# Performance work log

Measured on AMD Instinct MI355X. Metric: run time of the kernel, lower is better.

The kernel has to match this reference:

```python
import jax, jax.numpy as jnp
import numpy as np

EPS = 1e-5
NUM_HEADS = 8


def _conv_transpose_3x3_s2(x, w):
    # x: [B,Cin,H,W], w: [Cin,Cout,3,3] (torch ConvTranspose2d layout), stride 2, no padding
    # output spatial = (H-1)*2 + 3 = 2H+1
    return jax.lax.conv_transpose(
        x, w, strides=(2, 2), padding='VALID',
        dimension_numbers=('NCHW', 'IOHW', 'NCHW'))


def setup_inputs() -> dict:
    key = jax.random.key(0)
    ks = jax.random.split(key, 8)
    B, C, H, W = 4, 256, 32, 32
    Co, Dk, Dv = 128, 64, 64
    s = 0.05
    return {
        'x': jax.random.normal(ks[0], (B, C, H, W), jnp.float32),
        'gamma': jnp.ones((C,), jnp.float32),
        'beta': jnp.zeros((C,), jnp.float32),
        'running_mean': jax.random.normal(ks[1], (C,), jnp.float32) * 0.1,
        'running_var': jax.random.uniform(ks[2], (C,), jnp.float32, 0.5, 1.5),
        'w_sc': jax.random.normal(ks[3], (C, Co, 3, 3), jnp.float32) * s,
        'w_q': jax.random.normal(ks[4], (C, Dk, 3, 3), jnp.float32) * s,
        'w_k': jax.random.normal(ks[5], (Dk, C), jnp.float32) * s,
        'w_v': jax.random.normal(ks[6], (Dv, C), jnp.float32) * s,
        'w_o': jax.random.normal(ks[7], (Co, Dv), jnp.float32) * s,
    }


def reference(x, gamma, beta, running_mean, running_var, w_sc, w_q, w_k, w_v, w_o):
    B, C, H, W = x.shape
    h = NUM_HEADS
    # BatchNorm (inference, running stats) + ReLU, shared by both branches
    inv = jax.lax.rsqrt(running_var + EPS)
    xn = (x - running_mean[None, :, None, None]) * (gamma * inv)[None, :, None, None] \
         + beta[None, :, None, None]
    xr = jax.nn.relu(xn)

    # Shortcut: ConvTranspose2d(C->Co, 3, stride 2) -> [B,Co,2H+1,2W+1]
    shortcut = _conv_transpose_3x3_s2(xr, w_sc)

    # Attention branch ('UP'): query upsampled via ConvTranspose, k/v 1x1 at low res
    q = _conv_transpose_3x3_s2(xr, w_q)              # [B,Dk,Hu,Wu]
    k = jnp.einsum('dc,bchw->bdhw', w_k, xr)         # [B,Dk,H,W]
    v = jnp.einsum('dc,bchw->bdhw', w_v, xr)         # [B,Dv,H,W]
    Hu, Wu = q.shape[2], q.shape[3]
    Nq, Nk = Hu * Wu, H * W
    Dk, Dv = q.shape[1], v.shape[1]
    dk = Dk // h
    qh = q.reshape(B, h, dk, Nq)
    kh = k.reshape(B, h, dk, Nk)
    vh = v.reshape(B, h, Dv // h, Nk)
    scores = jnp.einsum('bhdq,bhdk->bhqk', qh, kh) / jnp.sqrt(jnp.float32(dk))
    attn = jax.nn.softmax(scores, axis=-1)           # use_softmax=True
    out = jnp.einsum('bhqk,bhdk->bhdq', attn, vh)    # [B,h,dv,Nq]
    out = out.reshape(B, Dv, Hu, Wu)
    out = jnp.einsum('od,bdhw->bohw', w_o, out)      # 1x1 output projection -> Co

    return shortcut + out
```

## Files before the change

kernel.cpp:

```cpp
#include <hip/hip_runtime.h>

typedef unsigned short u16;
typedef unsigned int u32;

typedef float f4 __attribute__((ext_vector_type(4)));
typedef short s8v __attribute__((ext_vector_type(8)));
typedef u16 us8 __attribute__((ext_vector_type(8)));
typedef _Float16 h4 __attribute__((ext_vector_type(4)));
typedef __fp16 g2 __attribute__((ext_vector_type(2)));

__device__ __forceinline__ u16 f2bf(float x){ u32 b=__float_as_uint(x); b += 0x7FFFu + ((b>>16)&1u); return (u16)(b>>16); }
__device__ __forceinline__ u16 f2h(float x){ union{_Float16 h; u16 u;} c; c.h=(_Float16)x; return c.u; }

#define O_XRT  4096u
#define O_WPT  (O_XRT + 2367488u)
#define O_QH   (O_WPT + 884736u)
#define O_KT   (O_QH  + 2163200u)
#define O_V    (O_KT  + 524288u)
#define O_ATT  (O_V   + 524288u)
#define O_WKV  (O_ATT + 2163200u)
#define O_WO2  (O_WKV + 65536u)

__global__ __launch_bounds__(256) void k_prep(
    const float* __restrict__ x, const float* __restrict__ gamma, const float* __restrict__ beta,
    const float* __restrict__ mean, const float* __restrict__ var,
    const float* __restrict__ w_sc, const float* __restrict__ w_q,
    const float* __restrict__ w_k, const float* __restrict__ w_v, const float* __restrict__ w_o,
    u16* __restrict__ xrTp, u16* __restrict__ wpt,
    u16* __restrict__ wkv, u16* __restrict__ wo2)
{
  __shared__ float SS[128], SH[128];
  __shared__ __align__(16) u16 T[32*136];
  int bi = blockIdx.x, tid = threadIdx.x;
  if (bi < 256) {
    int b = bi >> 6, pt = (bi >> 1) & 31, ch = bi & 1;
    int pix0 = pt*32, c0 = ch*128;
    if (tid < 128) {
      int c = c0 + tid;
      float s = gamma[c]*rsqrtf(var[c] + 1e-5f);
      SS[tid] = s; SH[tid] = beta[c] - mean[c]*s;
    }
    __syncthreads();
    int pix_l = tid & 31, c_l = tid >> 5;
    #pragma unroll 4
    for (int it = 0; it < 16; ++it) {
      int cl = it*8 + c_l;
      float v = x[(((size_t)(b*256 + c0 + cl))<<10) + pix0 + pix_l];
      T[pix_l*136 + cl] = f2bf(fmaxf(v*SS[cl] + SH[cl], 0.f));
    }
    __syncthreads();
    int pix_r = tid >> 3, j = tid & 7;
    us8 v0 = *(const us8*)(T + pix_r*136 + j*8);
    us8 v1 = *(const us8*)(T + pix_r*136 + 64 + j*8);
    u16* dst = xrTp + (((size_t)(b*1156 + (pt+1)*34 + 1 + pix_r))<<8) + c0;
    *(us8*)(dst + j*8) = v0;
    *(us8*)(dst + 64 + j*8) = v1;
    return;
  }
  int wid = (bi - 256)*256 + tid;
  if (wid < 442368) {
    int c, m, ky, kx; float val;
    if (wid < 294912) {
      c = wid / 1152; int r = wid - c*1152; m = r / 9; int t9 = r - m*9; ky = t9/3; kx = t9 - ky*3;
      val = w_sc[wid];
    } else {
      int i2 = wid - 294912;
      c = i2 / 576; int r = i2 - c*576; m = r / 9; int t9 = r - m*9; ky = t9/3; kx = t9 - ky*3;
      val = w_q[i2] * 0.51007023f;
      m += 128;
    }
    int py = (ky==1) ? 1 : 0; int dy = (ky==0) ? 1 : 0;
    int px = (kx==1) ? 1 : 0; int dx = (kx==0) ? 1 : 0;
    int cls = py*2 + px;
    int tt, KP, base;
    if (cls==0){ tt = dy*2+dx; KP=1024; base=0; }
    else if (cls==1){ tt = dy; KP=512; base=196608; }
    else if (cls==2){ tt = dx; KP=512; base=294912; }
    else { tt = 0; KP=256; base=393216; }
    wpt[base + m*KP + tt*256 + c] = f2bf(val);
  } else if (wid < 475136) {
    int i = wid - 442368; int m = i >> 8, c = i & 255;
    float vv = (m < 64) ? w_k[m*256 + c] : w_v[(m-64)*256 + c];
    wkv[m*256 + c] = f2bf(vv);
  } else if (wid < 483328) {
    int i = wid - 475136;
    wo2[i] = f2bf(w_o[i]);
  } else if (wid < 500224) {
    int i = wid - 483328;
    int b = i / 4224; int r = i - b*4224;
    int hp = r >> 5, j = r & 31;
    int p;
    if (hp < 34) p = hp;
    else if (hp < 68) p = 33*34 + (hp - 34);
    else if (hp < 100) p = (hp - 68 + 1)*34;
    else p = (hp - 100 + 1)*34 + 33;
    *(us8*)(xrTp + (((size_t)(b*1156 + p))<<8) + j*8) = (us8)0;
  }
}

template<int PY,int PX,int TT>
__device__ __forceinline__ void conv_cls(
    const u16* __restrict__ xrTp, const u16* __restrict__ wcls,
    float* __restrict__ outF, u16* __restrict__ qh,
    int mb, int nb, u16* Blds)
{
  constexpr int Hy = 33 - PY, Wx = 33 - PX;
  constexpr int NC = 4*Hy*Wx;
  constexpr int KP = TT*256;
  constexpr int NKT = KP/64;
  int tid = threadIdx.x;
  int lane = tid & 63, wv = tid >> 6, quad = lane >> 4, c15 = lane & 15;
  int sn = tid >> 2, sg = tid & 3;
  int n_g = nb*64 + sn;
  int ncl = n_g < NC ? n_g : NC-1;
  int bb = ncl/(Hy*Wx); int rem = ncl - bb*(Hy*Wx); int yq = rem/Wx; int xq = rem - yq*Wx;
  const u16* bsrc = xrTp + (((size_t)(bb*1156 + (yq+1)*34 + xq+1))<<8) + sg*16;
  f4 acc[4];
  #pragma unroll
  for (int i=0;i<4;i++) acc[i] = (f4){0.f,0.f,0.f,0.f};
  const u16* arow = wcls + (size_t)(mb*64 + wv*16 + c15)*KP + quad*8;
  auto loadB = [&](int kt, us8& v0, us8& v1) {
    int tt = kt >> 2, c0 = (kt & 3)*64;
    int dy, dx;
    if (TT==4){ dy = tt>>1; dx = tt&1; }
    else if (TT==2){ if (PX==1){ dy=tt; dx=0; } else { dy=0; dx=tt; } }
    else { dy=0; dx=0; }
    const u16* p = bsrc - (((dy*34+dx))<<8) + c0;
    v0 = *(const us8*)p;
    v1 = *(const us8*)(p+8);
  };
  us8 cv0, cv1; loadB(0, cv0, cv1);
  int pb = 0;
  for (int kt = 0; kt < NKT; ++kt) {
    u16* Bw = Blds + pb*4608;
    *(us8*)(Bw + sn*72 + sg*16) = cv0;
    *(us8*)(Bw + sn*72 + sg*16 + 8) = cv1;
    __syncthreads();
    if (kt + 1 < NKT) loadB(kt+1, cv0, cv1);
    s8v a0 = *(const s8v*)(arow + kt*64);
    s8v a1 = *(const s8v*)(arow + kt*64 + 32);
    #pragma unroll
    for (int t4=0;t4<4;t4++) {
      const u16* br = Blds + pb*4608 + (t4*16 + c15)*72 + quad*8;
      s8v bf0 = *(const s8v*)br;
      s8v bf1 = *(const s8v*)(br + 32);
      acc[t4] = __builtin_amdgcn_mfma_f32_16x16x32_bf16(a0, bf0, acc[t4], 0, 0, 0);
      acc[t4] = __builtin_amdgcn_mfma_f32_16x16x32_bf16(a1, bf1, acc[t4], 0, 0, 0);
    }
    pb ^= 1;
  }
  #pragma unroll
  for (int t4=0;t4<4;t4++) {
    int n2 = nb*64 + t4*16 + c15;
    if (n2 < NC) {
      int bb2 = n2/(Hy*Wx); int rem2 = n2 - bb2*(Hy*Wx); int yq2 = rem2/Wx; int xq2 = rem2 - yq2*Wx;
      int pix = (2*yq2 + PY)*65 + (2*xq2 + PX);
      if (mb < 2) {
        int mrow = mb*64 + wv*16 + quad*4;
        #pragma unroll
        for (int rg=0; rg<4; rg++)
          outF[(size_t)(bb2*128 + mrow + rg)*4225 + pix] = acc[t4][rg];
      } else {
        int dv = wv*16 + quad*4;
        u16 pk[4];
        #pragma unroll
        for (int rg=0; rg<4; rg++) pk[rg] = f2h(acc[t4][rg]);
        *(uint2*)(qh + (((size_t)(bb2*4225 + pix))<<6) + dv) = *(uint2*)pk;
      }
    }
  }
}

__global__ __launch_bounds__(256) void k_conv(
    const u16* __restrict__ xrTp, const u16* __restrict__ wpt, const u16* __restrict__ wkv,
    float* __restrict__ outF, u16* __restrict__ qh,
    u16* __restrict__ kT, u16* __restrict__ vbuf)
{
  __shared__ __align__(16) u16 Blds[2*4608];
  int bi = blockIdx.x;
  if (bi < 795) {
    int mb = bi % 3, cy = bi / 3;
    if (cy < 69)       conv_cls<0,0,4>(xrTp, wpt,          outF, qh, mb, cy,     Blds);
    else if (cy < 135) conv_cls<0,1,2>(xrTp, wpt + 196608, outF, qh, mb, cy-69,  Blds);
    else if (cy < 201) conv_cls<1,0,2>(xrTp, wpt + 294912, outF, qh, mb, cy-135, Blds);
    else               conv_cls<1,1,1>(xrTp, wpt + 393216, outF, qh, mb, cy-201, Blds);
    return;
  }
  int t = bi - 795;
  int mb = t & 1, nb = t >> 1;
  int tid = threadIdx.x;
  int lane = tid & 63, wv = tid >> 6, quad = lane >> 4, c15 = lane & 15;
  int sn = tid >> 2, sg = tid & 3;
  int n_g = nb*64 + sn;
  int b0 = n_g >> 10, pix0 = n_g & 1023, y0 = pix0 >> 5, x0 = pix0 & 31;
  const u16* bsrc = xrTp + (((size_t)(b0*1156 + (y0+1)*34 + x0+1))<<8) + sg*16;
  f4 acc[4];
  #pragma unroll
  for (int i=0;i<4;i++) acc[i] = (f4){0.f,0.f,0.f,0.f};
  const u16* arow = wkv + (size_t)(mb*64 + wv*16 + c15)*256 + quad*8;
  us8 cv0 = *(const us8*)bsrc, cv1 = *(const us8*)(bsrc + 8);
  int pb = 0;
  for (int kt = 0; kt < 4; ++kt) {
    u16* Bw = Blds + pb*4608;
    *(us8*)(Bw + sn*72 + sg*16) = cv0;
    *(us8*)(Bw + sn*72 + sg*16 + 8) = cv1;
    __syncthreads();
    if (kt < 3) { cv0 = *(const us8*)(bsrc + (kt+1)*64); cv1 = *(const us8*)(bsrc + (kt+1)*64 + 8); }
    s8v a0 = *(const s8v*)(arow + kt*64);
    s8v a1 = *(const s8v*)(arow + kt*64 + 32);
    #pragma unroll
    for (int t4=0;t4<4;t4++) {
      const u16* br = Blds + pb*4608 + (t4*16 + c15)*72 + quad*8;
      s8v bf0 = *(const s8v*)br;
      s8v bf1 = *(const s8v*)(br + 32);
      acc[t4] = __builtin_amdgcn_mfma_f32_16x16x32_bf16(a0, bf0, acc[t4], 0, 0, 0);
      acc[t4] = __builtin_amdgcn_mfma_f32_16x16x32_bf16(a1, bf1, acc[t4], 0, 0, 0);
    }
    pb ^= 1;
  }
  int ml = wv*16 + quad*4;
  #pragma unroll
  for (int t4=0;t4<4;t4++) {
    int n2 = nb*64 + t4*16 + c15;
    int b = n2 >> 10, pix = n2 & 1023;
    if (mb == 0) {
      int h = ml >> 3, d0 = ml & 7;
      u16 pk[4];
      #pragma unroll
      for (int rg=0; rg<4; rg++) pk[rg] = f2h(acc[t4][rg]);
      *(uint2*)(kT + ((size_t)(b*8+h)<<13) + pix*8 + d0) = *(uint2*)pk;
    } else {
      #pragma unroll
      for (int rg=0; rg<4; rg++)
        vbuf[(((size_t)(b*64 + ml + rg))<<10) + pix] = f2h(acc[t4][rg]);
    }
  }
}

__global__ __launch_bounds__(256) void k_attn(
    const u16* __restrict__ qh, const u16* __restrict__ kT, const u16* __restrict__ vbuf,
    u16* __restrict__ attT)
{
  __shared__ __align__(16) u16 KL[8192];
  __shared__ __align__(16) u16 VL[9*1032];
  int qt = blockIdx.x, bh = blockIdx.y;
  int b = bh >> 3, h = bh & 7;
  int tid = threadIdx.x, lane = tid & 63, wv = tid >> 6, quad = lane >> 4, c15 = lane & 15;
  {
    const uint4* kg = (const uint4*)(kT + ((size_t)bh << 13));
    for (int i = tid; i < 1024; i += 256) ((uint4*)KL)[i] = kg[i];
    const u16* vg = vbuf + ((size_t)(b*64 + h*8) << 10);
    for (int i = tid; i < 1024; i += 256) {
      int dv = i >> 7, k8 = (i & 127) << 3;
      *(uint4*)(VL + dv*1032 + k8) = *(const uint4*)(vg + (dv<<10) + k8);
    }
    if (tid < 129) {
      us8 ones;
      #pragma unroll
      for (int i=0;i<8;i++) ones[i] = 0x3C00;
      *(us8*)(VL + 8*1032 + tid*8) = ones;
    }
  }
  __syncthreads();
  int q0 = qt*128 + wv*32 + c15;
  int q1 = q0 + 16;
  int qa = q0 < 4224 ? q0 : 4224;
  int qb = q1 < 4224 ? q1 : 4224;
  uint2 t0 = *(const uint2*)(qh + (((size_t)(b*4225 + qa))<<6) + h*8 + (quad&1)*4);
  uint2 t1 = *(const uint2*)(qh + (((size_t)(b*4225 + qb))<<6) + h*8 + (quad&1)*4);
  h4 bq0 = quad < 2 ? *(h4*)&t0 : (h4)(_Float16)0.f;
  h4 bq1 = quad < 2 ? *(h4*)&t1 : (h4)(_Float16)0.f;
  const u16* klb = KL + c15*8 + (quad&1)*4;
  int vr = c15 > 8 ? 8 : c15;
  const u16* vlb = VL + vr*1032 + quad*4;
  const f4 zf = {0.f,0.f,0.f,0.f};
  f4 O0 = {0.f,0.f,0.f,0.f}, O1 = {0.f,0.f,0.f,0.f};
  union HU { uint2 u; h4 h; };
  #pragma unroll 8
  for (int kt=0; kt<64; ++kt) {
    h4 ak = *(const h4*)(klb + kt*128);
    h4 av = *(const h4*)(vlb + kt*16);
    f4 s0 = __builtin_amdgcn_mfma_f32_16x16x16f16(ak, bq0, zf, 0, 0, 0);
    f4 s1 = __builtin_amdgcn_mfma_f32_16x16x16f16(ak, bq1, zf, 0, 0, 0);
    g2 p0l = __builtin_amdgcn_cvt_pkrtz(__builtin_amdgcn_exp2f(s0[0]), __builtin_amdgcn_exp2f(s0[1]));
    g2 p0h = __builtin_amdgcn_cvt_pkrtz(__builtin_amdgcn_exp2f(s0[2]), __builtin_amdgcn_exp2f(s0[3]));
    g2 p1l = __builtin_amdgcn_cvt_pkrtz(__builtin_amdgcn_exp2f(s1[0]), __builtin_amdgcn_exp2f(s1[1]));
    g2 p1h = __builtin_amdgcn_cvt_pkrtz(__builtin_amdgcn_exp2f(s1[2]), __builtin_amdgcn_exp2f(s1[3]));
    HU u0; u0.u.x = __builtin_bit_cast(u32, p0l); u0.u.y = __builtin_bit_cast(u32, p0h);
    HU u1; u1.u.x = __builtin_bit_cast(u32, p1l); u1.u.y = __builtin_bit_cast(u32, p1h);
    O0 = __builtin_amdgcn_mfma_f32_16x16x16f16(av, u0.h, O0, 0, 0, 0);
    O1 = __builtin_amdgcn_mfma_f32_16x16x16f16(av, u1.h, O1, 0, 0, 0);
  }
  float l0 = __shfl(O0[0], 32 + c15, 64);
  float l1 = __shfl(O1[0], 32 + c15, 64);
  float r0 = __builtin_amdgcn_rcpf(l0);
  float r1 = __builtin_amdgcn_rcpf(l1);
  if (quad < 2) {
    if (q0 < 4225) {
      u16 pk[4];
      #pragma unroll
      for (int rg=0;rg<4;rg++) pk[rg] = f2bf(O0[rg]*r0);
      *(uint2*)(attT + (((size_t)(b*4225 + q0))<<6) + h*8 + quad*4) = *(uint2*)pk;
    }
    if (q1 < 4225) {
      u16 pk[4];
      #pragma unroll
      for (int rg=0;rg<4;rg++) pk[rg] = f2bf(O1[rg]*r1);
      *(uint2*)(attT + (((size_t)(b*4225 + q1))<<6) + h*8 + quad*4) = *(uint2*)pk;
    }
  }
}

__global__ __launch_bounds__(256) void k_proj(
    const u16* __restrict__ attT, const u16* __restrict__ wo2, float* __restrict__ outF)
{
  int nbi = blockIdx.x, b = blockIdx.y;
  int tid = threadIdx.x;
  int lane = tid & 63, wv = tid >> 6, quad = lane >> 4, c15 = lane & 15;
  f4 acc[2][4];
  #pragma unroll
  for (int am=0;am<2;am++)
    #pragma unroll
    for (int i=0;i<4;i++) acc[am][i] = (f4){0.f,0.f,0.f,0.f};
  #pragma unroll
  for (int kt = 0; kt < 2; ++kt) {
    s8v a0 = *(const s8v*)(wo2 + (size_t)(wv*32 + c15)*64 + kt*32 + quad*8);
    s8v a1 = *(const s8v*)(wo2 + (size_t)(wv*32 + 16 + c15)*64 + kt*32 + quad*8);
    #pragma unroll
    for (int t4=0;t4<4;t4++) {
      int n = nbi*64 + t4*16 + c15;
      int nc = n < 4224 ? n : 4224;
      s8v bf = *(const s8v*)(attT + (((size_t)(b*4225 + nc))<<6) + kt*32 + quad*8);
      acc[0][t4] = __builtin_amdgcn_mfma_f32_16x16x32_bf16(a0, bf, acc[0][t4], 0, 0, 0);
      acc[1][t4] = __builtin_amdgcn_mfma_f32_16x16x32_bf16(a1, bf, acc[1][t4], 0, 0, 0);
    }
  }
  #pragma unroll
  for (int am=0;am<2;am++) {
    int mrow = wv*32 + am*16 + quad*4;
    #pragma unroll
    for (int t4=0;t4<4;t4++) {
      int n2 = nbi*64 + t4*16 + c15;
      if (n2 < 4225) {
        float* op = outF + (size_t)(b*128 + mrow)*4225 + n2;
        #pragma unroll
        for (int rg=0; rg<4; rg++) op[(size_t)rg*4225] += acc[am][t4][rg];
      }
    }
  }
}

extern "C" void kernel_launch(void* const* d_in, const int* in_sizes, int n_in,
                              void* d_out, int out_size, void* d_ws, size_t ws_size,
                              hipStream_t stream) {
  const float* x     = (const float*)d_in[0];
  const float* gamma = (const float*)d_in[1];
  const float* beta  = (const float*)d_in[2];
  const float* mean  = (const float*)d_in[3];
  const float* var   = (const float*)d_in[4];
  const float* w_sc  = (const float*)d_in[5];
  const float* w_q   = (const float*)d_in[6];
  const float* w_k   = (const float*)d_in[7];
  const float* w_v   = (const float*)d_in[8];
  const float* w_o   = (const float*)d_in[9];
  char* ws = (char*)d_ws;
  u16*   xrTp = (u16*)(ws + O_XRT);
  u16*   wpt  = (u16*)(ws + O_WPT);
  u16*   qhb  = (u16*)(ws + O_QH);
  u16*   kT   = (u16*)(ws + O_KT);
  u16*   vbuf = (u16*)(ws + O_V);
  u16*   attT = (u16*)(ws + O_ATT);
  u16*   wkv  = (u16*)(ws + O_WKV);
  u16*   wo2  = (u16*)(ws + O_WO2);
  float* outF = (float*)d_out;

  k_prep<<<2211, 256, 0, stream>>>(x, gamma, beta, mean, var, w_sc, w_q, w_k, w_v, w_o,
                                   xrTp, wpt, wkv, wo2);
  k_conv<<<923, 256, 0, stream>>>(xrTp, wpt, wkv, outF, qhb, kT, vbuf);
  k_attn<<<dim3(34, 32), 256, 0, stream>>>(qhb, kT, vbuf, attT);
  k_proj<<<dim3(67, 4), 256, 0, stream>>>(attT, wo2, outF);
}
```

Baseline: 135.5 us.

## Use 32x32x16 MFMA in conv kernels, split prep and proj for more blocks

The conv and k/v GEMM loops move from 16x16x32 MFMA tiles to 32x32x16 tiles arranged as a 2x2 wave grid. A-fragments are now prefetched one k-step ahead in registers. This is meant to cut LDS B-fragment reads per FLOP and improve MFMA efficiency, at the cost of more registers. Separately, the activation prep now handles 64 channels per block, giving twice as many blocks, and the output projection is split across two M-blocks to raise parallelism for these small kernels.

```diff
diff --git a/kernel.cpp b/kernel.cpp
--- a/kernel.cpp
+++ b/kernel.cpp
@@ -4,6 +4,7 @@
 typedef unsigned int u32;
 
 typedef float f4 __attribute__((ext_vector_type(4)));
+typedef float f16v __attribute__((ext_vector_type(16)));
 typedef short s8v __attribute__((ext_vector_type(8)));
 typedef u16 us8 __attribute__((ext_vector_type(8)));
 typedef _Float16 h4 __attribute__((ext_vector_type(4)));
@@ -29,35 +30,33 @@
     u16* __restrict__ xrTp, u16* __restrict__ wpt,
     u16* __restrict__ wkv, u16* __restrict__ wo2)
 {
-  __shared__ float SS[128], SH[128];
-  __shared__ __align__(16) u16 T[32*136];
+  __shared__ float SS[64], SH[64];
+  __shared__ __align__(16) u16 T[32*72];
   int bi = blockIdx.x, tid = threadIdx.x;
-  if (bi < 256) {
-    int b = bi >> 6, pt = (bi >> 1) & 31, ch = bi & 1;
-    int pix0 = pt*32, c0 = ch*128;
-    if (tid < 128) {
+  if (bi < 512) {
+    int b = bi >> 7, pt = (bi >> 2) & 31, ch = bi & 3;
+    int pix0 = pt*32, c0 = ch*64;
+    if (tid < 64) {
       int c = c0 + tid;
       float s = gamma[c]*rsqrtf(var[c] + 1e-5f);
       SS[tid] = s; SH[tid] = beta[c] - mean[c]*s;
     }
     __syncthreads();
     int pix_l = tid & 31, c_l = tid >> 5;
-    #pragma unroll 4
-    for (int it = 0; it < 16; ++it) {
+    #pragma unroll
+    for (int it = 0; it < 8; ++it) {
       int cl = it*8 + c_l;
       float v = x[(((size_t)(b*256 + c0 + cl))<<10) + pix0 + pix_l];
-      T[pix_l*136 + cl] = f2bf(fmaxf(v*SS[cl] + SH[cl], 0.f));
+      T[pix_l*72 + cl] = f2bf(fmaxf(v*SS[cl] + SH[cl], 0.f));
     }
     __syncthreads();
     int pix_r = tid >> 3, j = tid & 7;
-    us8 v0 = *(const us8*)(T + pix_r*136 + j*8);
-    us8 v1 = *(const us8*)(T + pix_r*136 + 64 + j*8);
+    us8 v0 = *(const us8*)(T + pix_r*72 + j*8);
     u16* dst = xrTp + (((size_t)(b*1156 + (pt+1)*34 + 1 + pix_r))<<8) + c0;
     *(us8*)(dst + j*8) = v0;
-    *(us8*)(dst + 64 + j*8) = v1;
     return;
   }
-  int wid = (bi - 256)*256 + tid;
+  int wid = (bi - 512)*256 + tid;
   if (wid < 442368) {
     int c, m, ky, kx; float val;
     if (wid < 294912) {
@@ -109,16 +108,16 @@
   constexpr int KP = TT*256;
   constexpr int NKT = KP/64;
   int tid = threadIdx.x;
-  int lane = tid & 63, wv = tid >> 6, quad = lane >> 4, c15 = lane & 15;
+  int lane = tid & 63, wv = tid >> 6;
+  int tm = wv & 1, tn = wv >> 1;
+  int n32 = lane & 31, kh = lane >> 5;
   int sn = tid >> 2, sg = tid & 3;
   int n_g = nb*64 + sn;
   int ncl = n_g < NC ? n_g : NC-1;
   int bb = ncl/(Hy*Wx); int rem = ncl - bb*(Hy*Wx); int yq = rem/Wx; int xq = rem - yq*Wx;
   const u16* bsrc = xrTp + (((size_t)(bb*1156 + (yq+1)*34 + xq+1))<<8) + sg*16;
-  f4 acc[4];
-  #pragma unroll
-  for (int i=0;i<4;i++) acc[i] = (f4){0.f,0.f,0.f,0.f};
-  const u16* arow = wcls + (size_t)(mb*64 + wv*16 + c15)*KP + quad*8;
+  f16v acc = (f16v)0.f;
+  const u16* arow = wcls + (size_t)(mb*64 + tm*32 + n32)*KP + kh*8;
   auto loadB = [&](int kt, us8& v0, us8& v1) {
     int tt = kt >> 2, c0 = (kt & 3)*64;
     int dy, dx;
@@ -130,41 +129,49 @@
     v1 = *(const us8*)(p+8);
   };
   us8 cv0, cv1; loadB(0, cv0, cv1);
+  s8v a[4], an[4];
+  #pragma unroll
+  for (int s=0;s<4;s++) a[s] = *(const s8v*)(arow + s*16);
   int pb = 0;
   for (int kt = 0; kt < NKT; ++kt) {
     u16* Bw = Blds + pb*4608;
     *(us8*)(Bw + sn*72 + sg*16) = cv0;
     *(us8*)(Bw + sn*72 + sg*16 + 8) = cv1;
     __syncthreads();
-    if (kt + 1 < NKT) loadB(kt+1, cv0, cv1);
-    s8v a0 = *(const s8v*)(arow + kt*64);
-    s8v a1 = *(const s8v*)(arow + kt*64 + 32);
-    #pragma unroll
-    for (int t4=0;t4<4;t4++) {
-      const u16* br = Blds + pb*4608 + (t4*16 + c15)*72 + quad*8;
-      s8v bf0 = *(const s8v*)br;
-      s8v bf1 = *(const s8v*)(br + 32);
-      acc[t4] = __builtin_amdgcn_mfma_f32_16x16x32_bf16(a0, bf0, acc[t4], 0, 0, 0);
-      acc[t4] = __builtin_amdgcn_mfma_f32_16x16x32_bf16(a1, bf1, acc[t4], 0, 0, 0);
-    }
+    if (kt + 1 < NKT) {
+      loadB(kt+1, cv0, cv1);
+      #pragma unroll
+      for (int s=0;s<4;s++) an[s] = *(const s8v*)(arow + (kt+1)*64 + s*16);
+    }
+    const u16* br = Blds + pb*4608 + (tn*32 + n32)*72 + kh*8;
+    #pragma unroll
+    for (int s=0;s<4;s++) {
+      s8v bf = *(const s8v*)(br + s*16);
+      acc = __builtin_amdgcn_mfma_f32_32x32x16_bf16(a[s], bf, acc, 0, 0, 0);
+    }
+    #pragma unroll
+    for (int s=0;s<4;s++) a[s] = an[s];
     pb ^= 1;
   }
-  #pragma unroll
-  for (int t4=0;t4<4;t4++) {
-    int n2 = nb*64 + t4*16 + c15;
-    if (n2 < NC) {
-      int bb2 = n2/(Hy*Wx); int rem2 = n2 - bb2*(Hy*Wx); int yq2 = rem2/Wx; int xq2 = rem2 - yq2*Wx;
-      int pix = (2*yq2 + PY)*65 + (2*xq2 + PX);
-      if (mb < 2) {
-        int mrow = mb*64 + wv*16 + quad*4;
+  int n2 = nb*64 + tn*32 + n32;
+  if (n2 < NC) {
+    int bb2 = n2/(Hy*Wx); int rem2 = n2 - bb2*(Hy*Wx); int yq2 = rem2/Wx; int xq2 = rem2 - yq2*Wx;
+    int pix = (2*yq2 + PY)*65 + (2*xq2 + PX);
+    if (mb < 2) {
+      #pragma unroll
+      for (int g=0; g<4; g++) {
+        int m0 = mb*64 + tm*32 + g*8 + kh*4;
         #pragma unroll
-        for (int rg=0; rg<4; rg++)
-          outF[(size_t)(bb2*128 + mrow + rg)*4225 + pix] = acc[t4][rg];
-      } else {
-        int dv = wv*16 + quad*4;
+        for (int r=0;r<4;r++)
+          outF[(size_t)(bb2*128 + m0 + r)*4225 + pix] = acc[g*4+r];
+      }
+    } else {
+      #pragma unroll
+      for (int g=0; g<4; g++) {
+        int dv = tm*32 + g*8 + kh*4;
         u16 pk[4];
         #pragma unroll
-        for (int rg=0; rg<4; rg++) pk[rg] = f2h(acc[t4][rg]);
+        for (int r=0;r<4;r++) pk[r] = f2h(acc[g*4+r]);
         *(uint2*)(qh + (((size_t)(bb2*4225 + pix))<<6) + dv) = *(uint2*)pk;
       }
     }
@@ -187,52 +194,57 @@
     return;
   }
   int t = bi - 795;
-  int mb = t & 1, nb = t >> 1;
+  int mb = t & 1, nbk = t >> 1;
   int tid = threadIdx.x;
-  int lane = tid & 63, wv = tid >> 6, quad = lane >> 4, c15 = lane & 15;
+  int lane = tid & 63, wv = tid >> 6;
+  int tm = wv & 1, tn = wv >> 1;
+  int n32 = lane & 31, kh = lane >> 5;
   int sn = tid >> 2, sg = tid & 3;
-  int n_g = nb*64 + sn;
+  int n_g = nbk*64 + sn;
   int b0 = n_g >> 10, pix0 = n_g & 1023, y0 = pix0 >> 5, x0 = pix0 & 31;
   const u16* bsrc = xrTp + (((size_t)(b0*1156 + (y0+1)*34 + x0+1))<<8) + sg*16;
-  f4 acc[4];
-  #pragma unroll
-  for (int i=0;i<4;i++) acc[i] = (f4){0.f,0.f,0.f,0.f};
-  const u16* arow = wkv + (size_t)(mb*64 + wv*16 + c15)*256 + quad*8;
+  f16v acc = (f16v)0.f;
+  const u16* arow = wkv + (size_t)(mb*64 + tm*32 + n32)*256 + kh*8;
   us8 cv0 = *(const us8*)bsrc, cv1 = *(const us8*)(bsrc + 8);
+  s8v a[4], an[4];
+  #pragma unroll
+  for (int s=0;s<4;s++) a[s] = *(const s8v*)(arow + s*16);
   int pb = 0;
   for (int kt = 0; kt < 4; ++kt) {
     u16* Bw = Blds + pb*4608;
     *(us8*)(Bw + sn*72 + sg*16) = cv0;
     *(us8*)(Bw + sn*72 + sg*16 + 8) = cv1;
     __syncthreads();
-    if (kt < 3) { cv0 = *(const us8*)(bsrc + (kt+1)*64); cv1 = *(const us8*)(bsrc + (kt+1)*64 + 8); }
-    s8v a0 = *(const s8v*)(arow + kt*64);
-    s8v a1 = *(const s8v*)(arow + kt*64 + 32);
-    #pragma unroll
-    for (int t4=0;t4<4;t4++) {
-      const u16* br = Blds + pb*4608 + (t4*16 + c15)*72 + quad*8;
-      s8v bf0 = *(const s8v*)br;
-      s8v bf1 = *(const s8v*)(br + 32);
-      acc[t4] = __builtin_amdgcn_mfma_f32_16x16x32_bf16(a0, bf0, acc[t4], 0, 0, 0);
-      acc[t4] = __builtin_amdgcn_mfma_f32_16x16x32_bf16(a1, bf1, acc[t4], 0, 0, 0);
-    }
+    if (kt < 3) {
+      cv0 = *(const us8*)(bsrc + (kt+1)*64); cv1 = *(const us8*)(bsrc + (kt+1)*64 + 8);
+      #pragma unroll
+      for (int s=0;s<4;s++) an[s] = *(const s8v*)(arow + (kt+1)*64 + s*16);
+    }
+    const u16* br = Blds + pb*4608 + (tn*32 + n32)*72 + kh*8;
+    #pragma unroll
+    for (int s=0;s<4;s++) {
+      s8v bf = *(const s8v*)(br + s*16);
+      acc = __builtin_amdgcn_mfma_f32_32x32x16_bf16(a[s], bf, acc, 0, 0, 0);
+    }
+    #pragma unroll
+    for (int s=0;s<4;s++) a[s] = an[s];
     pb ^= 1;
   }
-  int ml = wv*16 + quad*4;
-  #pragma unroll
-  for (int t4=0;t4<4;t4++) {
-    int n2 = nb*64 + t4*16 + c15;
-    int b = n2 >> 10, pix = n2 & 1023;
+  int n2 = nbk*64 + tn*32 + n32;
+  int b = n2 >> 10, pix = n2 & 1023;
+  #pragma unroll
+  for (int g=0; g<4; g++) {
+    int ml = tm*32 + g*8 + kh*4;
     if (mb == 0) {
       int h = ml >> 3, d0 = ml & 7;
       u16 pk[4];
       #pragma unroll
-      for (int rg=0; rg<4; rg++) pk[rg] = f2h(acc[t4][rg]);
+      for (int r=0; r<4; r++) pk[r] = f2h(acc[g*4+r]);
       *(uint2*)(kT + ((size_t)(b*8+h)<<13) + pix*8 + d0) = *(uint2*)pk;
     } else {
       #pragma unroll
-      for (int rg=0; rg<4; rg++)
-        vbuf[(((size_t)(b*64 + ml + rg))<<10) + pix] = f2h(acc[t4][rg]);
+      for (int r=0; r<4; r++)
+        vbuf[(((size_t)(b*64 + ml + r))<<10) + pix] = f2h(acc[g*4+r]);
     }
   }
 }
@@ -314,38 +326,31 @@
 __global__ __launch_bounds__(256) void k_proj(
     const u16* __restrict__ attT, const u16* __restrict__ wo2, float* __restrict__ outF)
 {
-  int nbi = blockIdx.x, b = blockIdx.y;
+  int nbi = blockIdx.x, mb = blockIdx.y, b = blockIdx.z;
   int tid = threadIdx.x;
   int lane = tid & 63, wv = tid >> 6, quad = lane >> 4, c15 = lane & 15;
-  f4 acc[2][4];
-  #pragma unroll
-  for (int am=0;am<2;am++)
-    #pragma unroll
-    for (int i=0;i<4;i++) acc[am][i] = (f4){0.f,0.f,0.f,0.f};
+  f4 acc[4];
+  #pragma unroll
+  for (int i=0;i<4;i++) acc[i] = (f4){0.f,0.f,0.f,0.f};
   #pragma unroll
   for (int kt = 0; kt < 2; ++kt) {
-    s8v a0 = *(const s8v*)(wo2 + (size_t)(wv*32 + c15)*64 + kt*32 + quad*8);
-    s8v a1 = *(const s8v*)(wo2 + (size_t)(wv*32 + 16 + c15)*64 + kt*32 + quad*8);
+    s8v a0 = *(const s8v*)(wo2 + (size_t)(mb*64 + wv*16 + c15)*64 + kt*32 + quad*8);
     #pragma unroll
     for (int t4=0;t4<4;t4++) {
       int n = nbi*64 + t4*16 + c15;
       int nc = n < 4224 ? n : 4224;
       s8v bf = *(const s8v*)(attT + (((size_t)(b*4225 + nc))<<6) + kt*32 + quad*8);
-      acc[0][t4] = __builtin_amdgcn_mfma_f32_16x16x32_bf16(a0, bf, acc[0][t4], 0, 0, 0);
-      acc[1][t4] = __builtin_amdgcn_mfma_f32_16x16x32_bf16(a1, bf, acc[1][t4], 0, 0, 0);
-    }
-  }
-  #pragma unroll
-  for (int am=0;am<2;am++) {
-    int mrow = wv*32 + am*16 + quad*4;
-    #pragma unroll
-    for (int t4=0;t4<4;t4++) {
-      int n2 = nbi*64 + t4*16 + c15;
-      if (n2 < 4225) {
-        float* op = outF + (size_t)(b*128 + mrow)*4225 + n2;
-        #pragma unroll
-        for (int rg=0; rg<4; rg++) op[(size_t)rg*4225] += acc[am][t4][rg];
-      }
+      acc[t4] = __builtin_amdgcn_mfma_f32_16x16x32_bf16(a0, bf, acc[t4], 0, 0, 0);
+    }
+  }
+  int mrow = mb*64 + wv*16 + quad*4;
+  #pragma unroll
+  for (int t4=0;t4<4;t4++) {
+    int n2 = nbi*64 + t4*16 + c15;
+    if (n2 < 4225) {
+      float* op = outF + (size_t)(b*128 + mrow)*4225 + n2;
+      #pragma unroll
+      for (int rg=0; rg<4; rg++) op[(size_t)rg*4225] += acc[t4][rg];
     }
   }
 }
@@ -374,9 +379,9 @@
   u16*   wo2  = (u16*)(ws + O_WO2);
   float* outF = (float*)d_out;
 
-  k_prep<<<2211, 256, 0, stream>>>(x, gamma, beta, mean, var, w_sc, w_q, w_k, w_v, w_o,
+  k_prep<<<2466, 256, 0, stream>>>(x, gamma, beta, mean, var, w_sc, w_q, w_k, w_v, w_o,
                                    xrTp, wpt, wkv, wo2);
   k_conv<<<923, 256, 0, stream>>>(xrTp, wpt, wkv, outF, qhb, kT, vbuf);
   k_attn<<<dim3(34, 32), 256, 0, stream>>>(qhb, kT, vbuf, attT);
-  k_proj<<<dim3(67, 4), 256, 0, stream>>>(attT, wo2, outF);
-}
+  k_proj<<<dim3(67, 2, 4), 256, 0, stream>>>(attT, wo2, outF);
+}
```

Measured after the change: 140.9 us. 4.0% more time.
